# Kernel tuning notes

Hardware: AMD Instinct MI355X
Metric: run time of the kernel (lower is better)

## Reference

```python
import jax, jax.numpy as jnp
import numpy as np

N_NODES = 100000
N_EDGES = 300000
N_GRAPHS = 2048
IN_DIM = 38
HID = 256
LAYERS = 5
OUT_DIM = 1
BN_EPS = 1e-5


def setup_inputs() -> dict:
    key = jax.random.key(0)
    ks = jax.random.split(key, 20)
    x = jax.random.normal(ks[0], (N_NODES, IN_DIM), dtype=jnp.float32)
    edge_index = jax.random.randint(ks[1], (2, N_EDGES), 0, N_NODES, dtype=jnp.int32)
    batch = jnp.sort(jax.random.randint(ks[2], (N_NODES,), 0, N_GRAPHS, dtype=jnp.int32))
    s_in = 1.0 / np.sqrt(IN_DIM)
    s_h = 1.0 / np.sqrt(HID)
    return {
        "x": x,
        "edge_index": edge_index,
        "batch": batch,
        "Wp": jax.random.uniform(ks[3], (IN_DIM, HID), jnp.float32, -s_in, s_in),
        "bp": jnp.zeros((HID,), jnp.float32),
        "eps": jnp.zeros((LAYERS,), jnp.float32),  # train_eps=True, init 0
        "W1s": jax.random.uniform(ks[4], (LAYERS, HID, HID), jnp.float32, -s_h, s_h),
        "b1s": jnp.zeros((LAYERS, HID), jnp.float32),
        "W2s": jax.random.uniform(ks[5], (LAYERS, HID, HID), jnp.float32, -s_h, s_h),
        "b2s": jnp.zeros((LAYERS, HID), jnp.float32),
        "gammas": jnp.ones((LAYERS, HID), jnp.float32),
        "betas": jnp.zeros((LAYERS, HID), jnp.float32),
        "Wr1": jax.random.uniform(ks[6], (HID, HID), jnp.float32, -s_h, s_h),
        "br1": jnp.zeros((HID,), jnp.float32),
        "Wr2": jax.random.uniform(ks[7], (HID, OUT_DIM), jnp.float32, -s_h, s_h),
        "br2": jnp.zeros((OUT_DIM,), jnp.float32),
    }


def _forward(x, edge_index, batch, Wp, bp, eps, W1s, b1s, W2s, b2s,
             gammas, betas, Wr1, br1, Wr2, br2):
    src, dst = edge_index[0], edge_index[1]
    h = x @ Wp + bp  # [N, HID]
    for l in range(LAYERS):
        # GINConv: (1+eps)*h_i + sum_{j->i} h_j  (scatter-add over edges)
        agg = jnp.zeros_like(h).at[dst].add(h[src])
        z = (1.0 + eps[l]) * h + agg
        # 2-layer MLP
        z = jax.nn.relu(z @ W1s[l] + b1s[l]) @ W2s[l] + b2s[l]
        # BatchNorm1d (training-mode batch statistics, biased variance)
        mu = jnp.mean(z, axis=0)
        var = jnp.var(z, axis=0)
        z = (z - mu) * jax.lax.rsqrt(var + BN_EPS) * gammas[l] + betas[l]
        h = jax.nn.relu(z)  # dropout disabled (eval)
    # global mean pool over graphs
    sums = jax.ops.segment_sum(h, batch, num_segments=N_GRAPHS)
    counts = jax.ops.segment_sum(jnp.ones((h.shape[0],), h.dtype), batch,
                                 num_segments=N_GRAPHS)
    pooled = sums / jnp.maximum(counts, 1.0)[:, None]
    # readout MLP (dropout disabled)
    out = jax.nn.relu(pooled @ Wr1 + br1) @ Wr2 + br2
    return out  # [N_GRAPHS, OUT_DIM]


def reference(x, edge_index, batch, Wp, bp, eps, W1s, b1s, W2s, b2s,
              gammas, betas, Wr1, br1, Wr2, br2):
    return _forward(x, edge_index, batch, Wp, bp, eps, W1s, b1s, W2s, b2s,
                    gammas, betas, Wr1, br1, Wr2, br2)
```

## Files before the change

### kernel.cpp

```cpp
#include <hip/hip_runtime.h>

#define N_NODES 100000
#define N_EDGES 300000
#define N_GRAPHS 2048
#define IN_DIM 38
#define HID 256
#define LAYERS 5
#define BN_EPS 1e-5f

#define SCAN_CHUNK 512
#define N_CHUNKS ((N_NODES + SCAN_CHUNK - 1) / SCAN_CHUNK)

#define ROW_PAD 128

typedef unsigned short u16;
typedef unsigned int u32;
typedef __attribute__((ext_vector_type(8))) short short8;
typedef __attribute__((ext_vector_type(4))) unsigned short ushortx4;
typedef __attribute__((ext_vector_type(4))) unsigned int uintx4;
typedef __attribute__((ext_vector_type(4))) float floatx4;

__device__ __forceinline__ unsigned short bf16_rne(float f) {
    unsigned int u = __float_as_uint(f);
    unsigned int r = (u + 0x7fffu + ((u >> 16) & 1u)) >> 16;
    return (unsigned short)r;
}
__device__ __forceinline__ float uf(unsigned short b) {
    return __uint_as_float((unsigned int)b << 16);
}
__device__ __forceinline__ float unpack_pair(u32 w) {
    return uf((unsigned short)(w & 0xffffu)) + uf((unsigned short)(w >> 16));
}
__device__ __forceinline__ void split_bf16(float v, unsigned short& hi,
                                           unsigned short& lo) {
    hi = bf16_rne(v);
    float hf = __uint_as_float((unsigned int)hi << 16);
    lo = (unsigned short)(__float_as_uint(v - hf) >> 16);
}
__device__ __forceinline__ u32 pack_pair(float v) {
    unsigned short hb, lb;
    split_bf16(v, hb, lb);
    return (u32)hb | ((u32)lb << 16);
}
__device__ __forceinline__ int swz(int b) {
    return b ^ (((b >> 8) & 3) << 4) ^ (((b >> 12) & 1) << 6);
}
__device__ __forceinline__ void bn_params(const float* sums, const float* sumsq,
                                          const float* gammas,
                                          const float* betas, int c, float& sc,
                                          float& sh) {
    const float invN = 1.0f / (float)N_NODES;
    float mu = sums[c] * invN;
    float var = sumsq[c] * invN - mu * mu;
    float rs = rsqrtf(var + BN_EPS);
    float g = gammas[c];
    sc = rs * g;
    sh = betas[c] - mu * rs * g;
}

#define PROJ_CH 64
__global__ __launch_bounds__(256) void proj_kernel(
    const float* __restrict__ x, const float* __restrict__ Wp,
    const float* __restrict__ bp, u32* __restrict__ h) {
    __shared__ float xs[PROJ_CH * IN_DIM];
    int t = threadIdx.x;
    float w[IN_DIM];
#pragma unroll
    for (int k = 0; k < IN_DIM; k++) w[k] = Wp[k * HID + t];
    float b = bp[t];
    int n0 = blockIdx.x * PROJ_CH;
    int count = min(PROJ_CH, N_NODES - n0);
    int total = count * IN_DIM;
    const float* xbase = x + (size_t)n0 * IN_DIM;
    for (int i = t; i < total; i += 256) xs[i] = xbase[i];
    __syncthreads();
    for (int n = 0; n < count; n++) {
        float acc = b;
        const float* xr = &xs[n * IN_DIM];
#pragma unroll
        for (int k = 0; k < IN_DIM; k++) acc = fmaf(xr[k], w[k], acc);
        h[(size_t)(n0 + n) * 256 + t] = pack_pair(acc);
    }
}

__global__ __launch_bounds__(256) void hist_kernel(const int* __restrict__ ei,
                                                   int* __restrict__ deg) {
    int e = blockIdx.x * 256 + threadIdx.x;
    if (e < N_EDGES) atomicAdd(&deg[ei[N_EDGES + e]], 1);
}

__global__ __launch_bounds__(256) void scan1_kernel(const int* __restrict__ deg,
                                                    int* __restrict__ offs,
                                                    int* __restrict__ blocksums) {
    __shared__ int s[SCAN_CHUNK];
    int base = blockIdx.x * SCAN_CHUNK;
    int t = threadIdx.x;
    int i0 = t, i1 = t + 256;
    int g0 = base + i0, g1 = base + i1;
    int o0 = (g0 < N_NODES) ? deg[g0] : 0;
    int o1 = (g1 < N_NODES) ? deg[g1] : 0;
    s[i0] = o0;
    s[i1] = o1;
    __syncthreads();
    for (int off = 1; off < SCAN_CHUNK; off <<= 1) {
        int v0 = (i0 >= off) ? s[i0 - off] : 0;
        int v1 = (i1 >= off) ? s[i1 - off] : 0;
        __syncthreads();
        s[i0] += v0;
        s[i1] += v1;
        __syncthreads();
    }
    if (g0 < N_NODES) offs[g0] = s[i0] - o0;
    if (g1 < N_NODES) offs[g1] = s[i1] - o1;
    if (t == 0) blocksums[blockIdx.x] = s[SCAN_CHUNK - 1];
}

__global__ __launch_bounds__(256) void scan2_kernel(int* __restrict__ blocksums) {
    __shared__ int s[256];
    int t = threadIdx.x;
    int o = (t < N_CHUNKS) ? blocksums[t] : 0;
    s[t] = o;
    __syncthreads();
    for (int off = 1; off < 256; off <<= 1) {
        int v = (t >= off) ? s[t - off] : 0;
        __syncthreads();
        s[t] += v;
        __syncthreads();
    }
    if (t < N_CHUNKS) blocksums[t] = s[t] - o;
}

__global__ __launch_bounds__(256) void scan3_kernel(int* __restrict__ offs,
                                                    const int* __restrict__ blocksums,
                                                    int* __restrict__ cursor) {
    int g = blockIdx.x * 256 + threadIdx.x;
    if (g < N_NODES) {
        int v = offs[g] + blocksums[g / SCAN_CHUNK];
        offs[g] = v;
        cursor[g] = v;
    }
    if (g == 0) offs[N_NODES] = N_EDGES;
}

__global__ __launch_bounds__(256) void fill_kernel(const int* __restrict__ ei,
                                                   int* __restrict__ cursor,
                                                   int* __restrict__ csr_src) {
    int e = blockIdx.x * 256 + threadIdx.x;
    if (e < N_EDGES) {
        int src = ei[e];
        int dst = ei[N_EDGES + e];
        int pos = atomicAdd(&cursor[dst], 1);
        csr_src[pos] = src;
    }
}

__global__ __launch_bounds__(256) void packW_kernel(const float* __restrict__ W1s,
                                                    const float* __restrict__ W2s,
                                                    short8* __restrict__ Wpk8) {
    int id = blockIdx.x * 256 + threadIdx.x;
    int lane = id & 63;
    int fid = (id >> 6) & 127;
    int w = id >> 13;
    int kt = fid >> 4, nt = fid & 15;
    const float* Wsrc = (w < 5) ? W1s + (size_t)w * HID * HID
                                : W2s + (size_t)(w - 5) * HID * HID;
    int k0 = kt * 32 + ((lane >> 4) << 3);
    int n = nt * 16 + (lane & 15);
    short8 hi, lo;
#pragma unroll
    for (int e = 0; e < 8; e++) {
        float v = Wsrc[(size_t)(k0 + e) * HID + n];
        unsigned short hb, lb;
        split_bf16(v, hb, lb);
        hi[e] = (short)hb;
        lo[e] = (short)lb;
    }
    size_t base = (size_t)w * 16384;
    Wpk8[base + (size_t)((0 * 8 + kt) * 16 + nt) * 64 + lane] = hi;
    Wpk8[base + (size_t)((1 * 8 + kt) * 16 + nt) * 64 + lane] = lo;
}

__global__ __launch_bounds__(256, 2) void fused_mlp_kernel(
    const u32* __restrict__ zin, const int* __restrict__ offs,
    const int* __restrict__ csr_src, const float* __restrict__ eps, int layer,
    const float* __restrict__ psums, const float* __restrict__ psumsq,
    const float* __restrict__ pgam, const float* __restrict__ pbet, int useBN,
    const short8* __restrict__ W1m, const float* __restrict__ b1,
    const short8* __restrict__ W2m, const float* __restrict__ b2,
    u32* __restrict__ C, int M, float* __restrict__ sums,
    float* __restrict__ sumsq) {
    __shared__ char lds[65536];
    u16* Hf = (u16*)lds;
    float* cf = (float*)lds;
    int t = threadIdx.x;
    int lane = t & 63;
    int w = t >> 6;
    int m0 = blockIdx.x * 64;
    int col15 = lane & 15;
    int rgrp = lane >> 4;

    short8 bb[2][8];
    short8 aa[2][8];

    {
        float s = 1.0f + eps[layer];
        int c0 = lane * 4;
        float4 sc = make_float4(1.f, 1.f, 1.f, 1.f);
        float4 sh = make_float4(0.f, 0.f, 0.f, 0.f);
        if (useBN) {
            bn_params(psums, psumsq, pgam, pbet, c0 + 0, sc.x, sh.x);
            bn_params(psums, psumsq, pgam, pbet, c0 + 1, sc.y, sh.y);
            bn_params(psums, psumsq, pgam, pbet, c0 + 2, sc.z, sh.z);
            bn_params(psums, psumsq, pgam, pbet, c0 + 3, sc.w, sh.w);
        }
        int fb0 = ((lane >> 4) * 8 + ((lane >> 3) & 1) * 4 + w) * 1024 +
                  ((lane >> 1) & 3) * 256 + (lane & 1) * 8;
        for (int g = 0; g < 16; g++) {
            int node = m0 + w * 16 + g;
            float acc[4] = {0.f, 0.f, 0.f, 0.f};
            if (node < N_NODES) {
                int beg = offs[node], end = offs[node + 1];
                uintx4 vs = *(const uintx4*)&zin[(size_t)node * 256 + c0];
                acc[0] = unpack_pair(vs[0]);
                acc[1] = unpack_pair(vs[1]);
                acc[2] = unpack_pair(vs[2]);
                acc[3] = unpack_pair(vs[3]);
                if (useBN) {
                    acc[0] = fmaxf(acc[0] * sc.x + sh.x, 0.f);
                    acc[1] = fmaxf(acc[1] * sc.y + sh.y, 0.f);
                    acc[2] = fmaxf(acc[2] * sc.z + sh.z, 0.f);
                    acc[3] = fmaxf(acc[3] * sc.w + sh.w, 0.f);
                }
                acc[0] *= s; acc[1] *= s; acc[2] *= s; acc[3] *= s;
                for (int base = beg; base < end; base += 4) {
                    int i0 = csr_src[base];
                    int i1 = (base + 1 < end) ? csr_src[base + 1] : i0;
                    int i2 = (base + 2 < end) ? csr_src[base + 2] : i0;
                    int i3 = (base + 3 < end) ? csr_src[base + 3] : i0;
                    uintx4 r0 = *(const uintx4*)&zin[(size_t)i0 * 256 + c0];
                    uintx4 r1 = *(const uintx4*)&zin[(size_t)i1 * 256 + c0];
                    uintx4 r2 = *(const uintx4*)&zin[(size_t)i2 * 256 + c0];
                    uintx4 r3 = *(const uintx4*)&zin[(size_t)i3 * 256 + c0];
#define PROC_ROW(rv)                                                   \
                    {                                                  \
                        float v0 = unpack_pair(rv[0]);                 \
                        float v1 = unpack_pair(rv[1]);                 \
                        float v2 = unpack_pair(rv[2]);                 \
                        float v3 = unpack_pair(rv[3]);                 \
                        if (useBN) {                                   \
                            v0 = fmaxf(v0 * sc.x + sh.x, 0.f);         \
                            v1 = fmaxf(v1 * sc.y + sh.y, 0.f);         \
                            v2 = fmaxf(v2 * sc.z + sh.z, 0.f);         \
                            v3 = fmaxf(v3 * sc.w + sh.w, 0.f);         \
                        }                                              \
                        acc[0] += v0; acc[1] += v1;                    \
                        acc[2] += v2; acc[3] += v3;                    \
                    }
                    PROC_ROW(r0);
                    if (base + 1 < end) PROC_ROW(r1);
                    if (base + 2 < end) PROC_ROW(r2);
                    if (base + 3 < end) PROC_ROW(r3);
#undef PROC_ROW
                }
            }
            ushortx4 ho, lo2;
#pragma unroll
            for (int q = 0; q < 4; q++) {
                unsigned short hb, lb;
                split_bf16(acc[q], hb, lb);
                ho[q] = hb;
                lo2[q] = lb;
            }
            int sb = swz(fb0 + g * 16);
            *(ushortx4*)(lds + sb) = ho;
            *(ushortx4*)(lds + sb + 32768) = lo2;
        }
    }
#pragma unroll
    for (int q = 0; q < 8; q++) {
        int p = q >> 2, j = q & 3;
        bb[0][q] = W1m[((size_t)(p * 8 + 0) * 16 + (w * 4 + j)) * 64 + lane];
    }
    __syncthreads();

    floatx4 acc[4][4];
#pragma unroll
    for (int i = 0; i < 4; i++)
#pragma unroll
        for (int j = 0; j < 4; j++) acc[i][j] = (floatx4)0.0f;

#pragma unroll
    for (int q = 0; q < 8; q++) {
        int p = q >> 2, mt = q & 3;
        aa[0][q] = *(short8*)(lds + swz(((p * 32 + mt) * 64 + lane) * 16));
    }

#pragma unroll
    for (int kk = 0; kk < 8; kk++) {
        const int cur = kk & 1, nxt = cur ^ 1;
        if (kk < 7) {
#pragma unroll
            for (int q = 0; q < 8; q++) {
                int p = q >> 2, j = q & 3;
                bb[nxt][q] =
                    W1m[((size_t)(p * 8 + kk + 1) * 16 + (w * 4 + j)) * 64 + lane];
            }
#pragma unroll
            for (int q = 0; q < 8; q++) {
                int p = q >> 2, mt = q & 3;
                aa[nxt][q] = *(short8*)(
                    lds + swz(((p * 32 + (kk + 1) * 4 + mt) * 64 + lane) * 16));
            }
        }
        __builtin_amdgcn_s_setprio(1);
#pragma unroll
        for (int i = 0; i < 4; i++)
#pragma unroll
            for (int j = 0; j < 4; j++) {
                acc[i][j] = __builtin_amdgcn_mfma_f32_16x16x32_bf16(
                    aa[cur][i], bb[cur][j], acc[i][j], 0, 0, 0);
                acc[i][j] = __builtin_amdgcn_mfma_f32_16x16x32_bf16(
                    aa[cur][i], bb[cur][4 + j], acc[i][j], 0, 0, 0);
                acc[i][j] = __builtin_amdgcn_mfma_f32_16x16x32_bf16(
                    aa[cur][4 + i], bb[cur][j], acc[i][j], 0, 0, 0);
            }
        __builtin_amdgcn_s_setprio(0);
    }
    __syncthreads();

#pragma unroll
    for (int q = 0; q < 8; q++) {
        int p = q >> 2, j = q & 3;
        bb[0][q] = W2m[((size_t)(p * 8 + 0) * 16 + (w * 4 + j)) * 64 + lane];
    }
#pragma unroll
    for (int j = 0; j < 4; j++) {
        int col = w * 64 + j * 16 + col15;
        float bv = b1[col];
        int kt2 = col >> 5;
        int colg = (col & 31) >> 3;
        int e = col & 7;
#pragma unroll
        for (int i = 0; i < 4; i++) {
            int lane_a = rgrp * 4 + colg * 16;
#pragma unroll
            for (int r = 0; r < 4; r++) {
                float v = fmaxf(acc[i][j][r] + bv, 0.0f);
                unsigned short hb, lb;
                split_bf16(v, hb, lb);
                Hf[(((0 * 8 + kt2) * 4 + i) * 64 + lane_a + r) * 8 + e] = hb;
                Hf[(((1 * 8 + kt2) * 4 + i) * 64 + lane_a + r) * 8 + e] = lb;
            }
        }
    }
    __syncthreads();

    floatx4 acc2[4][4];
#pragma unroll
    for (int i = 0; i < 4; i++)
#pragma unroll
        for (int j = 0; j < 4; j++) acc2[i][j] = (floatx4)0.0f;

#pragma unroll
    for (int q = 0; q < 8; q++) {
        int p = q >> 2, mt = q & 3;
        aa[0][q] = *(short8*)&Hf[(((p * 8 + 0) * 4 + mt) * 64 + lane) * 8];
    }

#pragma unroll
    for (int kj = 0; kj < 8; kj++) {
        const int cur = kj & 1, nxt = cur ^ 1;
        if (kj < 7) {
#pragma unroll
            for (int q = 0; q < 8; q++) {
                int p = q >> 2, j = q & 3;
                bb[nxt][q] =
                    W2m[((size_t)(p * 8 + kj + 1) * 16 + (w * 4 + j)) * 64 + lane];
            }
#pragma unroll
            for (int q = 0; q < 8; q++) {
                int p = q >> 2, mt = q & 3;
                aa[nxt][q] =
                    *(short8*)&Hf[(((p * 8 + kj + 1) * 4 + mt) * 64 + lane) * 8];
            }
        }
        __builtin_amdgcn_s_setprio(1);
#pragma unroll
        for (int i = 0; i < 4; i++)
#pragma unroll
            for (int j = 0; j < 4; j++) {
                acc2[i][j] = __builtin_amdgcn_mfma_f32_16x16x32_bf16(
                    aa[cur][i], bb[cur][j], acc2[i][j], 0, 0, 0);
                acc2[i][j] = __builtin_amdgcn_mfma_f32_16x16x32_bf16(
                    aa[cur][i], bb[cur][4 + j], acc2[i][j], 0, 0, 0);
                acc2[i][j] = __builtin_amdgcn_mfma_f32_16x16x32_bf16(
                    aa[cur][4 + i], bb[cur][j], acc2[i][j], 0, 0, 0);
            }
        __builtin_amdgcn_s_setprio(0);
    }
    __syncthreads();

#pragma unroll
    for (int j = 0; j < 4; j++) {
        int col = w * 64 + j * 16 + col15;
        float bv = b2[col];
        float csum = 0.f, csq = 0.f;
#pragma unroll
        for (int i = 0; i < 4; i++) {
            int rowb = i * 16 + rgrp * 4;
#pragma unroll
            for (int r = 0; r < 4; r++) {
                float v = acc2[i][j][r] + bv;
                cf[(rowb + r) * 256 + col] = v;
                if (m0 + rowb + r < M) {
                    csum += v;
                    csq += v * v;
                }
            }
        }
        csum += __shfl_xor(csum, 16);
        csum += __shfl_xor(csum, 32);
        csq += __shfl_xor(csq, 16);
        csq += __shfl_xor(csq, 32);
        if (rgrp == 0) {
            atomicAdd(&sums[col], csum);
            atomicAdd(&sumsq[col], csq);
        }
    }
    __syncthreads();
#pragma unroll
    for (int k = 0; k < 16; k++) {
        int fi = (k * 256 + t) * 4;
        int row = fi >> 8, colc = fi & 255;
        int m = m0 + row;
        if (m >= M) continue;
        float4 v4 = *(float4*)&cf[fi];
        uintx4 o;
        o[0] = pack_pair(v4.x);
        o[1] = pack_pair(v4.y);
        o[2] = pack_pair(v4.z);
        o[3] = pack_pair(v4.w);
        *(uintx4*)&C[(size_t)m * 256 + colc] = o;
    }
}

__global__ __launch_bounds__(256) void bounds_kernel(const int* __restrict__ batch,
                                                     int* __restrict__ start) {
    int g = blockIdx.x * 256 + threadIdx.x;
    if (g > N_GRAPHS) return;
    int lo = 0, hi = N_NODES;
    while (lo < hi) {
        int mid = (lo + hi) >> 1;
        if (batch[mid] < g) lo = mid + 1;
        else hi = mid;
    }
    start[g] = lo;
}

__global__ __launch_bounds__(256) void segpool_kernel(
    const u32* __restrict__ z, const int* __restrict__ start,
    const float* __restrict__ sums, const float* __restrict__ sumsq,
    const float* __restrict__ gammas, const float* __restrict__ betas,
    float* __restrict__ pooled) {
    int g = blockIdx.x;
    int c = threadIdx.x;
    float sc, sh;
    bn_params(sums, sumsq, gammas, betas, c, sc, sh);
    int beg = start[g], end = start[g + 1];
    float s = 0.f;
    for (int n = beg; n < end; n++) {
        float v = unpack_pair(z[(size_t)n * 256 + c]);
        s += fmaxf(v * sc + sh, 0.f);
    }
    float inv = 1.0f / fmaxf((float)(end - beg), 1.0f);
    pooled[(size_t)g * HID + c] = s * inv;
}

#define RGK 8
__global__ __launch_bounds__(256) void readout_kernel(
    const float* __restrict__ pooled, const float* __restrict__ Wr1,
    const float* __restrict__ br1, const float* __restrict__ Wr2,
    const float* __restrict__ br2, float* __restrict__ out) {
    __shared__ float p[RGK][HID];
    __shared__ float red[RGK][4];
    int g0 = blockIdx.x * RGK;
    int t = threadIdx.x;
#pragma unroll
    for (int q = 0; q < RGK; q++) p[q][t] = pooled[(size_t)(g0 + q) * HID + t];
    __syncthreads();
    int c = t;
    float acc[RGK];
#pragma unroll
    for (int q = 0; q < RGK; q++) acc[q] = br1[c];
    for (int k = 0; k < HID; k++) {
        float wv = Wr1[k * HID + c];
#pragma unroll
        for (int q = 0; q < RGK; q++) acc[q] = fmaf(p[q][k], wv, acc[q]);
    }
    float w2 = Wr2[c];
#pragma unroll
    for (int q = 0; q < RGK; q++) {
        float v = fmaxf(acc[q], 0.f) * w2;
#pragma unroll
        for (int off = 32; off > 0; off >>= 1) v += __shfl_down(v, off, 64);
        if ((c & 63) == 0) red[q][c >> 6] = v;
    }
    __syncthreads();
    if (t < RGK)
        out[g0 + t] = red[t][0] + red[t][1] + red[t][2] + red[t][3] + br2[0];
}

extern "C" void kernel_launch(void* const* d_in, const int* in_sizes, int n_in,
                              void* d_out, int out_size, void* d_ws, size_t ws_size,
                              hipStream_t stream) {
    const float* x      = (const float*)d_in[0];
    const int*   ei     = (const int*)d_in[1];
    const int*   batch  = (const int*)d_in[2];
    const float* Wp     = (const float*)d_in[3];
    const float* bp     = (const float*)d_in[4];
    const float* eps    = (const float*)d_in[5];
    const float* W1s    = (const float*)d_in[6];
    const float* b1s    = (const float*)d_in[7];
    const float* W2s    = (const float*)d_in[8];
    const float* b2s    = (const float*)d_in[9];
    const float* gammas = (const float*)d_in[10];
    const float* betas  = (const float*)d_in[11];
    const float* Wr1    = (const float*)d_in[12];
    const float* br1    = (const float*)d_in[13];
    const float* Wr2    = (const float*)d_in[14];
    const float* br2    = (const float*)d_in[15];
    float* out = (float*)d_out;

    const size_t ROWS = (size_t)N_NODES + ROW_PAD;
    u32* bufA     = (u32*)d_ws;
    u32* bufC     = bufA + ROWS * 256;
    short8* Wpk8  = (short8*)(bufC + ROWS * 256);
    float* sums   = (float*)(Wpk8 + 10 * 16384);
    float* pooled = sums + LAYERS * 512;
    int* start     = (int*)(pooled + (size_t)N_GRAPHS * HID);
    int* deg       = start + N_GRAPHS + 1;
    int* offs      = deg + N_NODES;
    int* cursor    = offs + N_NODES + 1;
    int* csr_src   = cursor + N_NODES;
    int* blocksums = csr_src + N_EDGES;

    hipMemsetAsync(deg, 0, N_NODES * sizeof(int), stream);
    hipMemsetAsync(sums, 0, LAYERS * 512 * sizeof(float), stream);
    hist_kernel<<<(N_EDGES + 255) / 256, 256, 0, stream>>>(ei, deg);
    scan1_kernel<<<N_CHUNKS, 256, 0, stream>>>(deg, offs, blocksums);
    scan2_kernel<<<1, 256, 0, stream>>>(blocksums);
    scan3_kernel<<<(N_NODES + 255) / 256, 256, 0, stream>>>(offs, blocksums,
                                                            cursor);
    fill_kernel<<<(N_EDGES + 255) / 256, 256, 0, stream>>>(ei, cursor, csr_src);
    packW_kernel<<<320, 256, 0, stream>>>(W1s, W2s, Wpk8);
    bounds_kernel<<<(N_GRAPHS + 1 + 255) / 256, 256, 0, stream>>>(batch, start);

    proj_kernel<<<(N_NODES + PROJ_CH - 1) / PROJ_CH, 256, 0, stream>>>(x, Wp, bp,
                                                                       bufA);

    const int MLP_BLOCKS = (N_NODES + 63) / 64;
    u32* zin = bufA;
    u32* zout = bufC;
    for (int l = 0; l < LAYERS; l++) {
        float* lsums = sums + l * 512;
        float* lsumsq = lsums + 256;
        const float* psums = sums + (l - 1) * 512;
        fused_mlp_kernel<<<MLP_BLOCKS, 256, 0, stream>>>(
            zin, offs, csr_src, eps, l,
            l > 0 ? psums : sums, l > 0 ? psums + 256 : sums,
            gammas + (l > 0 ? (l - 1) : 0) * HID,
            betas + (l > 0 ? (l - 1) : 0) * HID, l > 0 ? 1 : 0,
            Wpk8 + (size_t)l * 16384, b1s + l * HID,
            Wpk8 + (size_t)(5 + l) * 16384, b2s + l * HID, zout, N_NODES,
            lsums, lsumsq);
        u32* tmp = zin; zin = zout; zout = tmp;
    }

    segpool_kernel<<<N_GRAPHS, 256, 0, stream>>>(
        zin, start, sums + 4 * 512, sums + 4 * 512 + 256, gammas + 4 * HID,
        betas + 4 * HID, pooled);
    readout_kernel<<<N_GRAPHS / RGK, 256, 0, stream>>>(pooled, Wr1, br1, Wr2, br2,
                                                       out);
}
```

Baseline: 1.124 ms.

## Halve MLP row tile to 32 and drop software double-buffering for higher occupancy

Shrinks each fused GIN MLP block from 64 to 32 node rows, halving LDS to 32KB and doubling the block count. It also raises launch bounds to 4 blocks per CU, and removes the register double-buffered prefetch of A/B fragments in favour of per-iteration loads. The aim is more resident waves to hide gather and global-weight latency. The cost is that each block reloads the full weight matrices for half as many rows, doubling weight traffic, and loads are no longer overlapped with MFMA within a wave.

Result: faster. 1.035 ms (-7.9%).

```diff
diff --git a/kernel.cpp b/kernel.cpp
--- a/kernel.cpp
+++ b/kernel.cpp
@@ -180,7 +180,7 @@
     Wpk8[base + (size_t)((1 * 8 + kt) * 16 + nt) * 64 + lane] = lo;
 }
 
-__global__ __launch_bounds__(256, 2) void fused_mlp_kernel(
+__global__ __launch_bounds__(256, 4) void fused_mlp_kernel(
     const u32* __restrict__ zin, const int* __restrict__ offs,
     const int* __restrict__ csr_src, const float* __restrict__ eps, int layer,
     const float* __restrict__ psums, const float* __restrict__ psumsq,
@@ -189,18 +189,15 @@
     const short8* __restrict__ W2m, const float* __restrict__ b2,
     u32* __restrict__ C, int M, float* __restrict__ sums,
     float* __restrict__ sumsq) {
-    __shared__ char lds[65536];
+    __shared__ char lds[32768];
     u16* Hf = (u16*)lds;
     float* cf = (float*)lds;
     int t = threadIdx.x;
     int lane = t & 63;
     int w = t >> 6;
-    int m0 = blockIdx.x * 64;
+    int m0 = blockIdx.x * 32;
     int col15 = lane & 15;
     int rgrp = lane >> 4;
-
-    short8 bb[2][8];
-    short8 aa[2][8];
 
     {
         float s = 1.0f + eps[layer];
@@ -213,10 +210,10 @@
             bn_params(psums, psumsq, pgam, pbet, c0 + 2, sc.z, sh.z);
             bn_params(psums, psumsq, pgam, pbet, c0 + 3, sc.w, sh.w);
         }
-        int fb0 = ((lane >> 4) * 8 + ((lane >> 3) & 1) * 4 + w) * 1024 +
-                  ((lane >> 1) & 3) * 256 + (lane & 1) * 8;
-        for (int g = 0; g < 16; g++) {
-            int node = m0 + w * 16 + g;
+        int fb0 = ((lane >> 3) * 2 + (w >> 1)) * 1024 + ((lane >> 1) & 3) * 256 +
+                  (lane & 1) * 8 + (w & 1) * 128;
+        for (int g = 0; g < 8; g++) {
+            int node = m0 + w * 8 + g;
             float acc[4] = {0.f, 0.f, 0.f, 0.f};
             if (node < N_NODES) {
                 int beg = offs[node], end = offs[node + 1];
@@ -273,66 +270,48 @@
             }
             int sb = swz(fb0 + g * 16);
             *(ushortx4*)(lds + sb) = ho;
-            *(ushortx4*)(lds + sb + 32768) = lo2;
-        }
-    }
-#pragma unroll
-    for (int q = 0; q < 8; q++) {
-        int p = q >> 2, j = q & 3;
-        bb[0][q] = W1m[((size_t)(p * 8 + 0) * 16 + (w * 4 + j)) * 64 + lane];
-    }
-    __syncthreads();
-
-    floatx4 acc[4][4];
-#pragma unroll
-    for (int i = 0; i < 4; i++)
+            *(ushortx4*)(lds + sb + 16384) = lo2;
+        }
+    }
+    __syncthreads();
+
+    floatx4 acc[2][4];
+#pragma unroll
+    for (int i = 0; i < 2; i++)
 #pragma unroll
         for (int j = 0; j < 4; j++) acc[i][j] = (floatx4)0.0f;
 
 #pragma unroll
-    for (int q = 0; q < 8; q++) {
-        int p = q >> 2, mt = q & 3;
-        aa[0][q] = *(short8*)(lds + swz(((p * 32 + mt) * 64 + lane) * 16));
-    }
-
-#pragma unroll
     for (int kk = 0; kk < 8; kk++) {
-        const int cur = kk & 1, nxt = cur ^ 1;
-        if (kk < 7) {
-#pragma unroll
-            for (int q = 0; q < 8; q++) {
-                int p = q >> 2, j = q & 3;
-                bb[nxt][q] =
-                    W1m[((size_t)(p * 8 + kk + 1) * 16 + (w * 4 + j)) * 64 + lane];
-            }
-#pragma unroll
-            for (int q = 0; q < 8; q++) {
-                int p = q >> 2, mt = q & 3;
-                aa[nxt][q] = *(short8*)(
-                    lds + swz(((p * 32 + (kk + 1) * 4 + mt) * 64 + lane) * 16));
-            }
+        short8 bb0[4], bb1[4];
+#pragma unroll
+        for (int j = 0; j < 4; j++) {
+            bb0[j] = W1m[((size_t)(0 * 8 + kk) * 16 + (w * 4 + j)) * 64 + lane];
+            bb1[j] = W1m[((size_t)(1 * 8 + kk) * 16 + (w * 4 + j)) * 64 + lane];
+        }
+        short8 ah[2], al[2];
+#pragma unroll
+        for (int mt = 0; mt < 2; mt++) {
+            int ib = swz(((kk * 2 + mt) * 64 + lane) * 16);
+            ah[mt] = *(short8*)(lds + ib);
+            al[mt] = *(short8*)(lds + ib + 16384);
         }
         __builtin_amdgcn_s_setprio(1);
 #pragma unroll
-        for (int i = 0; i < 4; i++)
+        for (int i = 0; i < 2; i++)
 #pragma unroll
             for (int j = 0; j < 4; j++) {
                 acc[i][j] = __builtin_amdgcn_mfma_f32_16x16x32_bf16(
-                    aa[cur][i], bb[cur][j], acc[i][j], 0, 0, 0);
+                    ah[i], bb0[j], acc[i][j], 0, 0, 0);
                 acc[i][j] = __builtin_amdgcn_mfma_f32_16x16x32_bf16(
-                    aa[cur][i], bb[cur][4 + j], acc[i][j], 0, 0, 0);
+                    ah[i], bb1[j], acc[i][j], 0, 0, 0);
                 acc[i][j] = __builtin_amdgcn_mfma_f32_16x16x32_bf16(
-                    aa[cur][4 + i], bb[cur][j], acc[i][j], 0, 0, 0);
+                    al[i], bb0[j], acc[i][j], 0, 0, 0);
             }
         __builtin_amdgcn_s_setprio(0);
     }
     __syncthreads();
 
-#pragma unroll
-    for (int q = 0; q < 8; q++) {
-        int p = q >> 2, j = q & 3;
-        bb[0][q] = W2m[((size_t)(p * 8 + 0) * 16 + (w * 4 + j)) * 64 + lane];
-    }
 #pragma unroll
     for (int j = 0; j < 4; j++) {
         int col = w * 64 + j * 16 + col15;
@@ -341,60 +320,52 @@
         int colg = (col & 31) >> 3;
         int e = col & 7;
 #pragma unroll
-        for (int i = 0; i < 4; i++) {
+        for (int i = 0; i < 2; i++) {
             int lane_a = rgrp * 4 + colg * 16;
 #pragma unroll
             for (int r = 0; r < 4; r++) {
                 float v = fmaxf(acc[i][j][r] + bv, 0.0f);
                 unsigned short hb, lb;
                 split_bf16(v, hb, lb);
-                Hf[(((0 * 8 + kt2) * 4 + i) * 64 + lane_a + r) * 8 + e] = hb;
-                Hf[(((1 * 8 + kt2) * 4 + i) * 64 + lane_a + r) * 8 + e] = lb;
+                Hf[(((0 * 8 + kt2) * 2 + i) * 64 + lane_a + r) * 8 + e] = hb;
+                Hf[(((1 * 8 + kt2) * 2 + i) * 64 + lane_a + r) * 8 + e] = lb;
             }
         }
     }
     __syncthreads();
 
-    floatx4 acc2[4][4];
-#pragma unroll
-    for (int i = 0; i < 4; i++)
+    floatx4 acc2[2][4];
+#pragma unroll
+    for (int i = 0; i < 2; i++)
 #pragma unroll
         for (int j = 0; j < 4; j++) acc2[i][j] = (floatx4)0.0f;
 
 #pragma unroll
-    for (int q = 0; q < 8; q++) {
-        int p = q >> 2, mt = q & 3;
-        aa[0][q] = *(short8*)&Hf[(((p * 8 + 0) * 4 + mt) * 64 + lane) * 8];
-    }
-
-#pragma unroll
     for (int kj = 0; kj < 8; kj++) {
-        const int cur = kj & 1, nxt = cur ^ 1;
-        if (kj < 7) {
-#pragma unroll
-            for (int q = 0; q < 8; q++) {
-                int p = q >> 2, j = q & 3;
-                bb[nxt][q] =
-                    W2m[((size_t)(p * 8 + kj + 1) * 16 + (w * 4 + j)) * 64 + lane];
-            }
-#pragma unroll
-            for (int q = 0; q < 8; q++) {
-                int p = q >> 2, mt = q & 3;
-                aa[nxt][q] =
-                    *(short8*)&Hf[(((p * 8 + kj + 1) * 4 + mt) * 64 + lane) * 8];
-            }
+        short8 bb2[2][4];
+#pragma unroll
+        for (int p = 0; p < 2; p++)
+#pragma unroll
+            for (int j = 0; j < 4; j++)
+                bb2[p][j] =
+                    W2m[((size_t)(p * 8 + kj) * 16 + (w * 4 + j)) * 64 + lane];
+        short8 ah2[2], al2[2];
+#pragma unroll
+        for (int mt = 0; mt < 2; mt++) {
+            ah2[mt] = *(short8*)&Hf[(((0 * 8 + kj) * 2 + mt) * 64 + lane) * 8];
+            al2[mt] = *(short8*)&Hf[(((1 * 8 + kj) * 2 + mt) * 64 + lane) * 8];
         }
         __builtin_amdgcn_s_setprio(1);
 #pragma unroll
-        for (int i = 0; i < 4; i++)
+        for (int i = 0; i < 2; i++)
 #pragma unroll
             for (int j = 0; j < 4; j++) {
                 acc2[i][j] = __builtin_amdgcn_mfma_f32_16x16x32_bf16(
-                    aa[cur][i], bb[cur][j], acc2[i][j], 0, 0, 0);
+                    ah2[i], bb2[0][j], acc2[i][j], 0, 0, 0);
                 acc2[i][j] = __builtin_amdgcn_mfma_f32_16x16x32_bf16(
-                    aa[cur][i], bb[cur][4 + j], acc2[i][j], 0, 0, 0);
+                    ah2[i], bb2[1][j], acc2[i][j], 0, 0, 0);
                 acc2[i][j] = __builtin_amdgcn_mfma_f32_16x16x32_bf16(
-                    aa[cur][4 + i], bb[cur][j], acc2[i][j], 0, 0, 0);
+                    al2[i], bb2[0][j], acc2[i][j], 0, 0, 0);
             }
         __builtin_amdgcn_s_setprio(0);
     }
@@ -406,7 +377,7 @@
         float bv = b2[col];
         float csum = 0.f, csq = 0.f;
 #pragma unroll
-        for (int i = 0; i < 4; i++) {
+        for (int i = 0; i < 2; i++) {
             int rowb = i * 16 + rgrp * 4;
 #pragma unroll
             for (int r = 0; r < 4; r++) {
@@ -429,7 +400,7 @@
     }
     __syncthreads();
 #pragma unroll
-    for (int k = 0; k < 16; k++) {
+    for (int k = 0; k < 8; k++) {
         int fi = (k * 256 + t) * 4;
         int row = fi >> 8, colc = fi & 255;
         int m = m0 + row;
@@ -558,7 +529,7 @@
     proj_kernel<<<(N_NODES + PROJ_CH - 1) / PROJ_CH, 256, 0, stream>>>(x, Wp, bp,
                                                                        bufA);
 
-    const int MLP_BLOCKS = (N_NODES + 63) / 64;
+    const int MLP_BLOCKS = (N_NODES + 31) / 32;
     u32* zin = bufA;
     u32* zout = bufC;
     for (int l = 0; l < LAYERS; l++) {
```
